# Performance work log

Hardware: AMD Instinct MI355X
Metric: run time of the kernel (lower is better)

Reference implementation:

```python
import jax, jax.numpy as jnp
import numpy as np
from jax import lax

N, CIN, P, CH, COUT = 1024, 3, 14, 256, 3
DN = ('NCHW', 'OIHW', 'NCHW')


def _conv(x, w, b, pad=1):
    y = lax.conv_general_dilated(x, w, (1, 1), [(pad, pad), (pad, pad)], dimension_numbers=DN)
    return y + b[None, :, None, None]


def _conv_transpose(x, w_t, b):
    # PyTorch ConvTranspose2d(k=3, stride=2, padding=1, output_padding=1):
    # equivalent to conv with lhs_dilation=2, padding (k-1-p, k-1-p+op) = (1, 2),
    # kernel with in/out swapped and spatially flipped. w_t: [in, out, 3, 3]
    w = jnp.flip(jnp.transpose(w_t, (1, 0, 2, 3)), axis=(2, 3))  # [out, in, 3, 3]
    y = lax.conv_general_dilated(x, w, (1, 1), [(1, 2), (1, 2)], lhs_dilation=(2, 2),
                                 dimension_numbers=DN)
    return y + b[None, :, None, None]


def setup_inputs() -> dict:
    key = jax.random.key(0)
    ks = jax.random.split(key, 16)
    s3 = lambda cin: 1.0 / np.sqrt(cin * 9)
    inp = {"x": jax.random.normal(ks[0], (N, CIN, P, P), dtype=jnp.float32)}
    inp["w1"] = jax.random.normal(ks[1], (CH, CIN, 3, 3), jnp.float32) * s3(CIN)
    inp["b1"] = jnp.zeros((CH,), jnp.float32)
    inp["w2"] = jax.random.normal(ks[2], (CH, CH, 3, 3), jnp.float32) * s3(CH)
    inp["b2"] = jnp.zeros((CH,), jnp.float32)
    inp["w3"] = jax.random.normal(ks[3], (CH, CH, 3, 3), jnp.float32) * s3(CH)
    inp["b3"] = jnp.zeros((CH,), jnp.float32)
    inp["w4"] = jax.random.normal(ks[4], (CH, CH, 3, 3), jnp.float32) * s3(CH)
    inp["b4"] = jnp.zeros((CH,), jnp.float32)
    inp["wt"] = jax.random.normal(ks[5], (CH, CH, 3, 3), jnp.float32) * s3(CH)  # [in, out, kh, kw]
    inp["bt"] = jnp.zeros((CH,), jnp.float32)
    inp["w5"] = jax.random.normal(ks[6], (COUT, CH, 1, 1), jnp.float32) * (1.0 / np.sqrt(CH))
    inp["b5"] = jnp.zeros((COUT,), jnp.float32)
    return inp


def reference(x, w1, b1, w2, b2, w3, b3, w4, b4, wt, bt, w5, b5):
    h = jax.nn.relu(_conv(x, w1, b1))
    h = jax.nn.relu(_conv(h, w2, b2))
    h = jax.nn.relu(_conv(h, w3, b3))
    h = jax.nn.relu(_conv(h, w4, b4))
    h = jax.nn.relu(_conv_transpose(h, wt, bt))  # [N, 256, 2P, 2P]
    h = _conv(h, w5, b5, pad=0)                   # 1x1 conv -> [N, 3, 2P, 2P]
    return jax.nn.sigmoid(h)
```

## Files before the change

kernel.cpp:

```cpp
#include <hip/hip_runtime.h>
#include <hip/hip_fp16.h>

typedef _Float16 half8 __attribute__((ext_vector_type(8)));
typedef _Float16 half4 __attribute__((ext_vector_type(4)));
typedef float floatx4 __attribute__((ext_vector_type(4)));

#define PLANE 65536
#define PK_ELEMS 589824

__global__ void repack_kernel(const float* __restrict__ w2, const float* __restrict__ w3,
                              const float* __restrict__ w4, const float* __restrict__ wt,
                              _Float16* __restrict__ pk) {
    int t = blockIdx.x * 256 + threadIdx.x;
    int l = t & 63;
    int idx = t >> 6;
    int nt = idx & 15; idx >>= 4;
    int ks = idx & 7;  idx >>= 3;
    int tap = idx % 9;
    int layer = idx / 9;
    int co = nt * 16 + (l & 15);
    int ci0 = ks * 32 + (l >> 4) * 8;
    const float* w = (layer == 0) ? w2 : (layer == 1) ? w3 : (layer == 2) ? w4 : wt;
    _Float16* dst = pk + (size_t)layer * PK_ELEMS + (((size_t)(tap * 8 + ks) * 16 + nt) * 64 + l) * 8;
    if (layer < 3) {
        for (int j = 0; j < 8; ++j)
            dst[j] = (_Float16)w[(co * 256 + (ci0 + j)) * 9 + tap];
    } else {
        int ky = tap / 3, kx = tap % 3;
        for (int j = 0; j < 8; ++j)
            dst[j] = (_Float16)w[((ci0 + j) * 256 + co) * 9 + (2 - ky) * 3 + (2 - kx)];
    }
}

__global__ __launch_bounds__(1024, 4) void conv1_kernel(const float* __restrict__ x,
                                                        const float* __restrict__ w1,
                                                        const float* __restrict__ b1,
                                                        _Float16* __restrict__ act) {
    __shared__ float inl[3][16][16];
    __shared__ float lw[256 * 27];
    __shared__ float lb1[256];
    int n = blockIdx.x, tid = threadIdx.x;
    if (tid < 768) ((float*)inl)[tid] = 0.f;
    __syncthreads();
    for (int i = tid; i < 3 * 196; i += 1024) {
        int ci = i / 196, r = i % 196, y = r / 14, xx = r % 14;
        inl[ci][y + 1][xx + 1] = x[(size_t)n * 588 + i];
    }
    for (int i = tid; i < 256 * 27; i += 1024) lw[i] = w1[i];
    if (tid < 256) lb1[tid] = b1[tid];
    __syncthreads();
    int p = tid >> 2, q = tid & 3;
    int py = p >> 4, px = p & 15;
    _Float16* ga = act + (size_t)n * PLANE + p * 256;
    int sw = (p & 7) << 3;
    if (py == 0 || py == 15 || px == 0 || px == 15) {
        for (int ci = 0; ci < 64; ++ci) { int co = q + ci * 4; ga[co ^ sw] = (_Float16)0.f; }
    } else {
        float vin[27];
        #pragma unroll
        for (int ci = 0; ci < 3; ++ci)
            #pragma unroll
            for (int ky = 0; ky < 3; ++ky)
                #pragma unroll
                for (int kx = 0; kx < 3; ++kx)
                    vin[ci * 9 + ky * 3 + kx] = inl[ci][py - 1 + ky][px - 1 + kx];
        for (int ci = 0; ci < 64; ++ci) {
            int co = q + ci * 4;
            float acc = lb1[co];
            const float* wp = &lw[co * 27];
            #pragma unroll
            for (int k = 0; k < 27; ++k) acc += vin[k] * wp[k];
            ga[co ^ sw] = (_Float16)fmaxf(acc, 0.f);
        }
    }
}


#define INIT_ACC(BIASPTR)                                                        \
    {                                                                            \
        _Pragma("unroll")                                                        \
        for (int ni = 0; ni < 4; ++ni) {                                         \
            floatx4 bv;                                                          \
            _Pragma("unroll")                                                    \
            for (int reg = 0; reg < 4; ++reg)                                    \
                bv[reg] = (BIASPTR)[(cg * 4 + ni) * 16 + kg * 4 + reg];          \
            _Pragma("unroll")                                                    \
            for (int i = 0; i < 5; ++i) acc[i][ni] = bv;                         \
        }                                                                        \
    }

#define ACCUM_TAP(PKT, DOFF)                                                     \
    {                                                                            \
        const _Float16* pkt_ = (PKT);                                            \
        int poff_[5];                                                            \
        _Pragma("unroll")                                                        \
        for (int j = 0; j < 5; ++j) poff_[j] = (pp[j] + (DOFF)) * 256;           \
        half8 a_[4], an_[4], bb_[5];                                             \
        _Pragma("unroll")                                                        \
        for (int ni = 0; ni < 4; ++ni)                                           \
            a_[ni] = *(const half8*)(pkt_ + ((cg * 4 + ni) * 64 + lane) * 8);    \
        _Pragma("clang loop unroll(disable)")                                    \
        for (int ks = 0; ks < 8; ++ks) {                                         \
            int kk = (ks * 4 + kg) << 3;                                         \
            _Pragma("unroll")                                                    \
            for (int j = 0; j < 4; ++j)                                          \
                bb_[j] = *(const half8*)(plane + poff_[j] + (kk ^ ((poff_[j] >> 5) & 56))); \
            if (pg == 0)                                                         \
                bb_[4] = *(const half8*)(plane + poff_[4] + (kk ^ ((poff_[4] >> 5) & 56))); \
            if (ks < 7) {                                                        \
                _Pragma("unroll")                                                \
                for (int ni = 0; ni < 4; ++ni)                                   \
                    an_[ni] = *(const half8*)(pkt_ + (((ks + 1) * 16 + cg * 4 + ni) * 64 + lane) * 8); \
            }                                                                    \
            _Pragma("unroll")                                                    \
            for (int j = 0; j < 4; ++j) {                                        \
                acc[j][0] = __builtin_amdgcn_mfma_f32_16x16x32_f16(a_[0], bb_[j], acc[j][0], 0, 0, 0); \
                acc[j][1] = __builtin_amdgcn_mfma_f32_16x16x32_f16(a_[1], bb_[j], acc[j][1], 0, 0, 0); \
                acc[j][2] = __builtin_amdgcn_mfma_f32_16x16x32_f16(a_[2], bb_[j], acc[j][2], 0, 0, 0); \
                acc[j][3] = __builtin_amdgcn_mfma_f32_16x16x32_f16(a_[3], bb_[j], acc[j][3], 0, 0, 0); \
            }                                                                    \
            if (pg == 0) {                                                       \
                acc[4][0] = __builtin_amdgcn_mfma_f32_16x16x32_f16(a_[0], bb_[4], acc[4][0], 0, 0, 0); \
                acc[4][1] = __builtin_amdgcn_mfma_f32_16x16x32_f16(a_[1], bb_[4], acc[4][1], 0, 0, 0); \
                acc[4][2] = __builtin_amdgcn_mfma_f32_16x16x32_f16(a_[2], bb_[4], acc[4][2], 0, 0, 0); \
                acc[4][3] = __builtin_amdgcn_mfma_f32_16x16x32_f16(a_[3], bb_[4], acc[4][3], 0, 0, 0); \
            }                                                                    \
            if (ks < 7) {                                                        \
                _Pragma("unroll")                                                \
                for (int ni = 0; ni < 4; ++ni) a_[ni] = an_[ni];                 \
            }                                                                    \
        }                                                                        \
    }

#define EPILOGUE(RY, RX)                                                         \
    {                                                                            \
        _Pragma("unroll")                                                        \
        for (int i = 0; i < 5; ++i) {                                            \
            if (i < 4 || pg == 0) {                                              \
                float s0 = 0.f, s1 = 0.f, s2 = 0.f;                              \
                _Pragma("unroll")                                                \
                for (int ni = 0; ni < 4; ++ni) {                                 \
                    int co0 = (cg * 4 + ni) * 16 + kg * 4;                       \
                    _Pragma("unroll")                                            \
                    for (int reg = 0; reg < 4; ++reg) {                          \
                        float v = fmaxf(acc[i][ni][reg], 0.f);                   \
                        s0 += v * w5l[co0 + reg];                                \
                        s1 += v * w5l[256 + co0 + reg];                          \
                        s2 += v * w5l[512 + co0 + reg];                          \
                    }                                                            \
                }                                                                \
                s0 += __shfl_xor(s0, 16, 64); s0 += __shfl_xor(s0, 32, 64);      \
                s1 += __shfl_xor(s1, 16, 64); s1 += __shfl_xor(s1, 32, 64);      \
                s2 += __shfl_xor(s2, 16, 64); s2 += __shfl_xor(s2, 32, 64);      \
                if (lane < 16 && pm[i] < 196) {                                  \
                    int yy = pm[i] / 14, xx2 = pm[i] - yy * 14;                  \
                    int pix = (2 * yy + (RY)) * 28 + 2 * xx2 + (RX);             \
                    atomicAdd(&o3[pix * 3 + 0], s0);                             \
                    atomicAdd(&o3[pix * 3 + 1], s1);                             \
                    atomicAdd(&o3[pix * 3 + 2], s2);                             \
                }                                                                \
            }                                                                    \
        }                                                                        \
    }

__global__ __launch_bounds__(768, 3) void fused_kernel(const _Float16* __restrict__ act,
                                                       const _Float16* __restrict__ pk,
                                                       const float* __restrict__ b2,
                                                       const float* __restrict__ b3,
                                                       const float* __restrict__ b4,
                                                       const float* __restrict__ bt,
                                                       const float* __restrict__ w5,
                                                       const float* __restrict__ b5,
                                                       float* __restrict__ out) {
    __shared__ _Float16 plane[PLANE];
    __shared__ float o3[2352];
    __shared__ float w5l[768];
    int n = blockIdx.x, tid = threadIdx.x;
    const _Float16* ga = act + (size_t)n * PLANE;
    for (int i = tid; i < 8192; i += 768)
        *(uint4*)(plane + i * 8) = *(const uint4*)(ga + i * 8);
    for (int i = tid; i < 2352; i += 768) o3[i] = b5[i % 3];
    w5l[tid] = w5[tid];

    int lane = tid & 63, wid = tid >> 6;
    int cg = wid & 3, pg = wid >> 2;
    int col = lane & 15, kg = lane >> 4;

    int pp[5], pm[5];
    #pragma unroll
    for (int i = 0; i < 5; ++i) {
        int m = (pg + 3 * i) * 16 + col;
        pm[i] = m;
        int mc = (m < 196) ? m : 195;
        int y = mc / 14, x = mc - y * 14;
        pp[i] = (y + 1) * 16 + x + 1;
    }
    __syncthreads();

    floatx4 acc[5][4];

    for (int L = 0; L < 3; ++L) {
        const _Float16* pkL = pk + (size_t)L * PK_ELEMS;
        const float* bias = (L == 0) ? b2 : (L == 1) ? b3 : b4;
        INIT_ACC(bias)
        for (int tap = 0; tap < 9; ++tap) {
            int doff = (tap / 3) * 16 + (tap % 3) - 17;
            ACCUM_TAP(pkL + (size_t)tap * 65536, doff)
        }
        __syncthreads();
        #pragma unroll
        for (int i = 0; i < 5; ++i) {
            if (i < 4 || pg == 0) {
                int ppix = pp[i];
                int sw = (ppix & 7) << 3;
                if (pm[i] < 196) {
                    #pragma unroll
                    for (int ni = 0; ni < 4; ++ni) {
                        int co0 = (cg * 4 + ni) * 16 + kg * 4;
                        half4 h;
                        #pragma unroll
                        for (int reg = 0; reg < 4; ++reg) h[reg] = (_Float16)fmaxf(acc[i][ni][reg], 0.f);
                        *(half4*)(plane + ppix * 256 + (co0 ^ sw)) = h;
                    }
                }
            }
        }
        __syncthreads();
    }

    const _Float16* pkT = pk + (size_t)3 * PK_ELEMS;
    INIT_ACC(bt)
    ACCUM_TAP(pkT + 4 * 65536, 0)
    EPILOGUE(0, 0)
    INIT_ACC(bt)
    ACCUM_TAP(pkT + 3 * 65536, 0)
    ACCUM_TAP(pkT + 5 * 65536, 1)
    EPILOGUE(0, 1)
    INIT_ACC(bt)
    ACCUM_TAP(pkT + 1 * 65536, 0)
    ACCUM_TAP(pkT + 7 * 65536, 16)
    EPILOGUE(1, 0)
    INIT_ACC(bt)
    ACCUM_TAP(pkT + 0 * 65536, 0)
    ACCUM_TAP(pkT + 2 * 65536, 1)
    ACCUM_TAP(pkT + 6 * 65536, 16)
    ACCUM_TAP(pkT + 8 * 65536, 17)
    EPILOGUE(1, 1)

    __syncthreads();
    size_t ob = (size_t)n * 2352;
    for (int i = tid; i < 2352; i += 768) {
        int pix = i / 3, c = i % 3;
        float v = o3[i];
        out[ob + (size_t)c * 784 + pix] = 1.f / (1.f + __expf(-v));
    }
}

extern "C" void kernel_launch(void* const* d_in, const int* in_sizes, int n_in,
                              void* d_out, int out_size, void* d_ws, size_t ws_size,
                              hipStream_t stream) {
    const float* x  = (const float*)d_in[0];
    const float* w1 = (const float*)d_in[1];
    const float* b1 = (const float*)d_in[2];
    const float* w2 = (const float*)d_in[3];
    const float* b2 = (const float*)d_in[4];
    const float* w3 = (const float*)d_in[5];
    const float* b3 = (const float*)d_in[6];
    const float* w4 = (const float*)d_in[7];
    const float* b4 = (const float*)d_in[8];
    const float* wt = (const float*)d_in[9];
    const float* bt = (const float*)d_in[10];
    const float* w5 = (const float*)d_in[11];
    const float* b5 = (const float*)d_in[12];

    size_t need = ((size_t)1024 * PLANE + 4 * (size_t)PK_ELEMS) * sizeof(_Float16);
    if (ws_size < need) return;

    _Float16* act = (_Float16*)d_ws;
    _Float16* pk  = act + (size_t)1024 * PLANE;

    repack_kernel<<<1152, 256, 0, stream>>>(w2, w3, w4, wt, pk);
    conv1_kernel<<<1024, 1024, 0, stream>>>(x, w1, b1, act);
    fused_kernel<<<1024, 768, 0, stream>>>(act, pk, b2, b3, b4, bt, w5, b5, (float*)d_out);
}
```

Before: 961.6 us.

## Map MMA N-tiles to padded image rows instead of packed pixels

Switches the pixel-to-MFMA-column mapping so each 16-wide N tile covers one padded 16-column image row, with guard bands of zeros added around the shared plane. This removes the per-pixel division/clamp index math and the wasted tail of partial tiles, and makes row-aligned, contiguous plane addressing. In exchange, 2 of the 16 columns per tile are padding (14 of 16 useful), so more MFMAs run: pg==1 waves now also execute a fifth tile, and shared memory grows by the guard regions, which may affect occupancy.

```diff
diff --git a/kernel.cpp b/kernel.cpp
--- a/kernel.cpp
+++ b/kernel.cpp
@@ -7,6 +7,7 @@
 
 #define PLANE 65536
 #define PK_ELEMS 589824
+#define GUARD 4096
 
 __global__ void repack_kernel(const float* __restrict__ w2, const float* __restrict__ w3,
                               const float* __restrict__ w4, const float* __restrict__ wt,
@@ -105,7 +106,7 @@
             _Pragma("unroll")                                                    \
             for (int j = 0; j < 4; ++j)                                          \
                 bb_[j] = *(const half8*)(plane + poff_[j] + (kk ^ ((poff_[j] >> 5) & 56))); \
-            if (pg == 0)                                                         \
+            if (pg == 0 || pg == 1)                                              \
                 bb_[4] = *(const half8*)(plane + poff_[4] + (kk ^ ((poff_[4] >> 5) & 56))); \
             if (ks < 7) {                                                        \
                 _Pragma("unroll")                                                \
@@ -119,7 +120,7 @@
                 acc[j][2] = __builtin_amdgcn_mfma_f32_16x16x32_f16(a_[2], bb_[j], acc[j][2], 0, 0, 0); \
                 acc[j][3] = __builtin_amdgcn_mfma_f32_16x16x32_f16(a_[3], bb_[j], acc[j][3], 0, 0, 0); \
             }                                                                    \
-            if (pg == 0) {                                                       \
+            if (pg == 0 || pg == 1) {                                            \
                 acc[4][0] = __builtin_amdgcn_mfma_f32_16x16x32_f16(a_[0], bb_[4], acc[4][0], 0, 0, 0); \
                 acc[4][1] = __builtin_amdgcn_mfma_f32_16x16x32_f16(a_[1], bb_[4], acc[4][1], 0, 0, 0); \
                 acc[4][2] = __builtin_amdgcn_mfma_f32_16x16x32_f16(a_[2], bb_[4], acc[4][2], 0, 0, 0); \
@@ -136,7 +137,7 @@
     {                                                                            \
         _Pragma("unroll")                                                        \
         for (int i = 0; i < 5; ++i) {                                            \
-            if (i < 4 || pg == 0) {                                              \
+            if (i < 4 || pg < 2) {                                               \
                 float s0 = 0.f, s1 = 0.f, s2 = 0.f;                              \
                 _Pragma("unroll")                                                \
                 for (int ni = 0; ni < 4; ++ni) {                                 \
@@ -152,9 +153,9 @@
                 s0 += __shfl_xor(s0, 16, 64); s0 += __shfl_xor(s0, 32, 64);      \
                 s1 += __shfl_xor(s1, 16, 64); s1 += __shfl_xor(s1, 32, 64);      \
                 s2 += __shfl_xor(s2, 16, 64); s2 += __shfl_xor(s2, 32, 64);      \
-                if (lane < 16 && pm[i] < 196) {                                  \
-                    int yy = pm[i] / 14, xx2 = pm[i] - yy * 14;                  \
-                    int pix = (2 * yy + (RY)) * 28 + 2 * xx2 + (RX);             \
+                if (lane < 16 && colok) {                                        \
+                    int yy = pg + 3 * i;                              \
+                    int pix = (2 * yy + (RY)) * 28 + 2 * (col - 1) + (RX);       \
                     atomicAdd(&o3[pix * 3 + 0], s0);                             \
                     atomicAdd(&o3[pix * 3 + 1], s1);                             \
                     atomicAdd(&o3[pix * 3 + 2], s2);                             \
@@ -172,29 +173,28 @@
                                                        const float* __restrict__ w5,
                                                        const float* __restrict__ b5,
                                                        float* __restrict__ out) {
-    __shared__ _Float16 plane[PLANE];
+    __shared__ _Float16 plane[PLANE + 2 * GUARD];
     __shared__ float o3[2352];
     __shared__ float w5l[768];
     int n = blockIdx.x, tid = threadIdx.x;
     const _Float16* ga = act + (size_t)n * PLANE;
+    if (tid < 512) {
+        int g = (tid < 256) ? tid : (tid - 256 + (PLANE + GUARD) / 8);
+        *(uint4*)(plane + g * 8) = uint4{0, 0, 0, 0};
+    }
     for (int i = tid; i < 8192; i += 768)
-        *(uint4*)(plane + i * 8) = *(const uint4*)(ga + i * 8);
+        *(uint4*)(plane + GUARD + i * 8) = *(const uint4*)(ga + i * 8);
     for (int i = tid; i < 2352; i += 768) o3[i] = b5[i % 3];
     w5l[tid] = w5[tid];
 
     int lane = tid & 63, wid = tid >> 6;
     int cg = wid & 3, pg = wid >> 2;
     int col = lane & 15, kg = lane >> 4;
-
-    int pp[5], pm[5];
+    bool colok = (col >= 1 && col <= 14);
+
+    int pp[5];
     #pragma unroll
-    for (int i = 0; i < 5; ++i) {
-        int m = (pg + 3 * i) * 16 + col;
-        pm[i] = m;
-        int mc = (m < 196) ? m : 195;
-        int y = mc / 14, x = mc - y * 14;
-        pp[i] = (y + 1) * 16 + x + 1;
-    }
+    for (int i = 0; i < 5; ++i) pp[i] = (pg + 3 * i + 1) * 16 + col + 16;
     __syncthreads();
 
     floatx4 acc[5][4];
@@ -210,10 +210,10 @@
         __syncthreads();
         #pragma unroll
         for (int i = 0; i < 5; ++i) {
-            if (i < 4 || pg == 0) {
+            if (i < 4 || pg < 2) {
                 int ppix = pp[i];
                 int sw = (ppix & 7) << 3;
-                if (pm[i] < 196) {
+                if (colok) {
                     #pragma unroll
                     for (int ni = 0; ni < 4; ++ni) {
                         int co0 = (cg * 4 + ni) * 16 + kg * 4;
```

Measured after the change: 1.026 ms. 6.6% more time.

## Use 16 waves with row-aligned pixel tiles and MFMA priority boost

Applied to the files above, without the earlier changes.

Raises the fused kernel from 12 to 16 waves per block and tiles pixels by image rows (14 valid of 16 columns), so each wave holds 4 pixel tiles instead of 5 and per-thread accumulator registers shrink. It drops the A-operand double-buffer prefetch, loading weights inline each k-step, and wraps the MFMA block in s_setprio to favour matrix issue. The row tiling wastes 2 of 16 columns per tile and the launch bound tightens register budget, while losing the software prefetch may expose global load latency.

```diff
diff --git a/kernel.cpp b/kernel.cpp
--- a/kernel.cpp
+++ b/kernel.cpp
@@ -85,58 +85,54 @@
             for (int reg = 0; reg < 4; ++reg)                                    \
                 bv[reg] = (BIASPTR)[(cg * 4 + ni) * 16 + kg * 4 + reg];          \
             _Pragma("unroll")                                                    \
-            for (int i = 0; i < 5; ++i) acc[i][ni] = bv;                         \
+            for (int i = 0; i < 4; ++i) acc[i][ni] = bv;                         \
         }                                                                        \
     }
 
 #define ACCUM_TAP(PKT, DOFF)                                                     \
     {                                                                            \
         const _Float16* pkt_ = (PKT);                                            \
-        int poff_[5];                                                            \
+        int poff_[4], swj_[4];                                                   \
         _Pragma("unroll")                                                        \
-        for (int j = 0; j < 5; ++j) poff_[j] = (pp[j] + (DOFF)) * 256;           \
-        half8 a_[4], an_[4], bb_[5];                                             \
-        _Pragma("unroll")                                                        \
-        for (int ni = 0; ni < 4; ++ni)                                           \
-            a_[ni] = *(const half8*)(pkt_ + ((cg * 4 + ni) * 64 + lane) * 8);    \
+        for (int j = 0; j < 4; ++j) {                                            \
+            poff_[j] = (pp[j] + (DOFF)) * 256;                                   \
+            swj_[j] = (poff_[j] >> 5) & 56;                                      \
+        }                                                                        \
+        half8 a_[4], b_[4];                                                      \
         _Pragma("clang loop unroll(disable)")                                    \
         for (int ks = 0; ks < 8; ++ks) {                                         \
-            int kk = (ks * 4 + kg) << 3;                                         \
-            _Pragma("unroll")                                                    \
-            for (int j = 0; j < 4; ++j)                                          \
-                bb_[j] = *(const half8*)(plane + poff_[j] + (kk ^ ((poff_[j] >> 5) & 56))); \
-            if (pg == 0)                                                         \
-                bb_[4] = *(const half8*)(plane + poff_[4] + (kk ^ ((poff_[4] >> 5) & 56))); \
-            if (ks < 7) {                                                        \
-                _Pragma("unroll")                                                \
-                for (int ni = 0; ni < 4; ++ni)                                   \
-                    an_[ni] = *(const half8*)(pkt_ + (((ks + 1) * 16 + cg * 4 + ni) * 64 + lane) * 8); \
+            int kk_ = (ks * 4 + kg) << 3;                                        \
+            b_[0] = *(const half8*)(plane + poff_[0] + (kk_ ^ swj_[0]));         \
+            b_[1] = *(const half8*)(plane + poff_[1] + (kk_ ^ swj_[1]));         \
+            b_[2] = *(const half8*)(plane + poff_[2] + (kk_ ^ swj_[2]));         \
+            if (t4)                                                              \
+                b_[3] = *(const half8*)(plane + poff_[3] + (kk_ ^ swj_[3]));     \
+            _Pragma("unroll")                                                    \
+            for (int ni = 0; ni < 4; ++ni)                                       \
+                a_[ni] = *(const half8*)(pkt_ + ((ks * 16 + cg * 4 + ni) * 64 + lane) * 8); \
+            __builtin_amdgcn_s_setprio(1);                                       \
+            _Pragma("unroll")                                                    \
+            for (int j = 0; j < 3; ++j) {                                        \
+                acc[j][0] = __builtin_amdgcn_mfma_f32_16x16x32_f16(a_[0], b_[j], acc[j][0], 0, 0, 0); \
+                acc[j][1] = __builtin_amdgcn_mfma_f32_16x16x32_f16(a_[1], b_[j], acc[j][1], 0, 0, 0); \
+                acc[j][2] = __builtin_amdgcn_mfma_f32_16x16x32_f16(a_[2], b_[j], acc[j][2], 0, 0, 0); \
+                acc[j][3] = __builtin_amdgcn_mfma_f32_16x16x32_f16(a_[3], b_[j], acc[j][3], 0, 0, 0); \
             }                                                                    \
-            _Pragma("unroll")                                                    \
-            for (int j = 0; j < 4; ++j) {                                        \
-                acc[j][0] = __builtin_amdgcn_mfma_f32_16x16x32_f16(a_[0], bb_[j], acc[j][0], 0, 0, 0); \
-                acc[j][1] = __builtin_amdgcn_mfma_f32_16x16x32_f16(a_[1], bb_[j], acc[j][1], 0, 0, 0); \
-                acc[j][2] = __builtin_amdgcn_mfma_f32_16x16x32_f16(a_[2], bb_[j], acc[j][2], 0, 0, 0); \
-                acc[j][3] = __builtin_amdgcn_mfma_f32_16x16x32_f16(a_[3], bb_[j], acc[j][3], 0, 0, 0); \
+            if (t4) {                                                            \
+                acc[3][0] = __builtin_amdgcn_mfma_f32_16x16x32_f16(a_[0], b_[3], acc[3][0], 0, 0, 0); \
+                acc[3][1] = __builtin_amdgcn_mfma_f32_16x16x32_f16(a_[1], b_[3], acc[3][1], 0, 0, 0); \
+                acc[3][2] = __builtin_amdgcn_mfma_f32_16x16x32_f16(a_[2], b_[3], acc[3][2], 0, 0, 0); \
+                acc[3][3] = __builtin_amdgcn_mfma_f32_16x16x32_f16(a_[3], b_[3], acc[3][3], 0, 0, 0); \
             }                                                                    \
-            if (pg == 0) {                                                       \
-                acc[4][0] = __builtin_amdgcn_mfma_f32_16x16x32_f16(a_[0], bb_[4], acc[4][0], 0, 0, 0); \
-                acc[4][1] = __builtin_amdgcn_mfma_f32_16x16x32_f16(a_[1], bb_[4], acc[4][1], 0, 0, 0); \
-                acc[4][2] = __builtin_amdgcn_mfma_f32_16x16x32_f16(a_[2], bb_[4], acc[4][2], 0, 0, 0); \
-                acc[4][3] = __builtin_amdgcn_mfma_f32_16x16x32_f16(a_[3], bb_[4], acc[4][3], 0, 0, 0); \
-            }                                                                    \
-            if (ks < 7) {                                                        \
-                _Pragma("unroll")                                                \
-                for (int ni = 0; ni < 4; ++ni) a_[ni] = an_[ni];                 \
-            }                                                                    \
+            __builtin_amdgcn_s_setprio(0);                                       \
         }                                                                        \
     }
 
 #define EPILOGUE(RY, RX)                                                         \
     {                                                                            \
         _Pragma("unroll")                                                        \
-        for (int i = 0; i < 5; ++i) {                                            \
-            if (i < 4 || pg == 0) {                                              \
+        for (int i = 0; i < 4; ++i) {                                            \
+            if (i < 3 || t4) {                                                   \
                 float s0 = 0.f, s1 = 0.f, s2 = 0.f;                              \
                 _Pragma("unroll")                                                \
                 for (int ni = 0; ni < 4; ++ni) {                                 \
@@ -152,9 +148,9 @@
                 s0 += __shfl_xor(s0, 16, 64); s0 += __shfl_xor(s0, 32, 64);      \
                 s1 += __shfl_xor(s1, 16, 64); s1 += __shfl_xor(s1, 32, 64);      \
                 s2 += __shfl_xor(s2, 16, 64); s2 += __shfl_xor(s2, 32, 64);      \
-                if (lane < 16 && pm[i] < 196) {                                  \
-                    int yy = pm[i] / 14, xx2 = pm[i] - yy * 14;                  \
-                    int pix = (2 * yy + (RY)) * 28 + 2 * xx2 + (RX);             \
+                if (lane < 14) {                                                 \
+                    int yy = pg + 4 * i;                                         \
+                    int pix = (2 * yy + (RY)) * 28 + 2 * lane + (RX);            \
                     atomicAdd(&o3[pix * 3 + 0], s0);                             \
                     atomicAdd(&o3[pix * 3 + 1], s1);                             \
                     atomicAdd(&o3[pix * 3 + 2], s2);                             \
@@ -163,41 +159,45 @@
         }                                                                        \
     }
 
-__global__ __launch_bounds__(768, 3) void fused_kernel(const _Float16* __restrict__ act,
-                                                       const _Float16* __restrict__ pk,
-                                                       const float* __restrict__ b2,
-                                                       const float* __restrict__ b3,
-                                                       const float* __restrict__ b4,
-                                                       const float* __restrict__ bt,
-                                                       const float* __restrict__ w5,
-                                                       const float* __restrict__ b5,
-                                                       float* __restrict__ out) {
+__global__ __launch_bounds__(1024, 4) void fused_kernel(const _Float16* __restrict__ act,
+                                                        const _Float16* __restrict__ pk,
+                                                        const float* __restrict__ b2,
+                                                        const float* __restrict__ b3,
+                                                        const float* __restrict__ b4,
+                                                        const float* __restrict__ bt,
+                                                        const float* __restrict__ w5,
+                                                        const float* __restrict__ b5,
+                                                        float* __restrict__ out) {
     __shared__ _Float16 plane[PLANE];
     __shared__ float o3[2352];
     __shared__ float w5l[768];
     int n = blockIdx.x, tid = threadIdx.x;
     const _Float16* ga = act + (size_t)n * PLANE;
-    for (int i = tid; i < 8192; i += 768)
-        *(uint4*)(plane + i * 8) = *(const uint4*)(ga + i * 8);
-    for (int i = tid; i < 2352; i += 768) o3[i] = b5[i % 3];
-    w5l[tid] = w5[tid];
-
-    int lane = tid & 63, wid = tid >> 6;
+    #pragma unroll
+    for (int i = 0; i < 8; ++i)
+        *(uint4*)(plane + (i * 1024 + tid) * 8) = *(const uint4*)(ga + (i * 1024 + tid) * 8);
+    for (int i = tid; i < 2352; i += 1024) o3[i] = b5[i % 3];
+    if (tid < 768) w5l[tid] = w5[tid];
+
+    int lane = tid & 63;
+    int wid = __builtin_amdgcn_readfirstlane(tid >> 6);
     int cg = wid & 3, pg = wid >> 2;
     int col = lane & 15, kg = lane >> 4;
-
-    int pp[5], pm[5];
-    #pragma unroll
-    for (int i = 0; i < 5; ++i) {
-        int m = (pg + 3 * i) * 16 + col;
-        pm[i] = m;
-        int mc = (m < 196) ? m : 195;
-        int y = mc / 14, x = mc - y * 14;
-        pp[i] = (y + 1) * 16 + x + 1;
-    }
-    __syncthreads();
-
-    floatx4 acc[5][4];
+    bool t4 = (pg < 2);
+
+    int pp[4];
+    {
+        int xc = (col < 14) ? col : 13;
+        #pragma unroll
+        for (int i = 0; i < 4; ++i) {
+            int rr = pg + 4 * i + 1; if (rr > 14) rr = 13;
+            pp[i] = rr * 16 + xc + 1;
+        }
+    }
+    bool colok = (col < 14);
+    __syncthreads();
+
+    floatx4 acc[4][4];
 
     for (int L = 0; L < 3; ++L) {
         const _Float16* pkL = pk + (size_t)L * PK_ELEMS;
@@ -209,19 +209,17 @@
         }
         __syncthreads();
         #pragma unroll
-        for (int i = 0; i < 5; ++i) {
-            if (i < 4 || pg == 0) {
+        for (int i = 0; i < 4; ++i) {
+            if ((i < 3 || t4) && colok) {
                 int ppix = pp[i];
                 int sw = (ppix & 7) << 3;
-                if (pm[i] < 196) {
+                #pragma unroll
+                for (int ni = 0; ni < 4; ++ni) {
+                    int co0 = (cg * 4 + ni) * 16 + kg * 4;
+                    half4 h;
                     #pragma unroll
-                    for (int ni = 0; ni < 4; ++ni) {
-                        int co0 = (cg * 4 + ni) * 16 + kg * 4;
-                        half4 h;
-                        #pragma unroll
-                        for (int reg = 0; reg < 4; ++reg) h[reg] = (_Float16)fmaxf(acc[i][ni][reg], 0.f);
-                        *(half4*)(plane + ppix * 256 + (co0 ^ sw)) = h;
-                    }
+                    for (int reg = 0; reg < 4; ++reg) h[reg] = (_Float16)fmaxf(acc[i][ni][reg], 0.f);
+                    *(half4*)(plane + ppix * 256 + (co0 ^ sw)) = h;
                 }
             }
         }
@@ -249,7 +247,7 @@
 
     __syncthreads();
     size_t ob = (size_t)n * 2352;
-    for (int i = tid; i < 2352; i += 768) {
+    for (int i = tid; i < 2352; i += 1024) {
         int pix = i / 3, c = i % 3;
         float v = o3[i];
         out[ob + (size_t)c * 784 + pix] = 1.f / (1.f + __expf(-v));
@@ -281,5 +279,5 @@
 
     repack_kernel<<<1152, 256, 0, stream>>>(w2, w3, w4, wt, pk);
     conv1_kernel<<<1024, 1024, 0, stream>>>(x, w1, b1, act);
-    fused_kernel<<<1024, 768, 0, stream>>>(act, pk, b2, b3, b4, bt, w5, b5, (float*)d_out);
-}
+    fused_kernel<<<1024, 1024, 0, stream>>>(act, pk, b2, b3, b4, bt, w5, b5, (float*)d_out);
+}
```

New measurement: 1.230 ms. +27.9%, slower.
